# Kernel tuning notes

Hardware: AMD Instinct MI355X
Metric: run time of the kernel (lower is better)

## Reference

```python
import jax, jax.numpy as jnp
import numpy as np

GROUP_SIZES = [2048, 4096, 8192, 16384]
TOP_K = 64
L1_COEFF = 1e-3
AUX_PENALTY = 1e-2
N_BATCHES_TO_DEAD = 20
AUX_K_MULT = 16


def setup_inputs() -> dict:
    D = 1024
    S = sum(GROUP_SIZES)  # 30720
    B = 2048
    key = jax.random.key(0)
    k1, k2, k3 = jax.random.split(key, 3)
    x = jax.random.normal(k1, (B, D), dtype=jnp.float32)
    # kaiming_uniform-like init for W_enc [D, S]
    bound = np.sqrt(6.0 / D)
    W_enc = jax.random.uniform(k2, (D, S), jnp.float32, -bound, bound)
    # W_dec = W_enc.T row-normalized (as in __init__)
    W_dec = W_enc.T
    W_dec = W_dec / jnp.linalg.norm(W_dec, axis=-1, keepdims=True)
    b_dec = jnp.zeros((D,), jnp.float32)
    b_enc = jnp.zeros((S,), jnp.float32)
    num_batches_not_active = jax.random.randint(k3, (S,), 0, 40, dtype=jnp.int32)
    return dict(x=x, b_dec=b_dec, b_enc=b_enc, W_enc=W_enc, W_dec=W_dec,
                num_batches_not_active=num_batches_not_active)


def reference(x, b_dec, b_enc, W_enc, W_dec, num_batches_not_active):
    B, D = x.shape
    S = W_enc.shape[1]
    # encoder
    acts = jax.nn.relu((x - b_dec) @ W_enc + b_enc)  # [B, S]
    # global (batch-level) top-k over flattened activations + scatter back
    k = TOP_K * B
    flat = acts.reshape(-1)
    vals, idx = jax.lax.top_k(flat, k)
    acts_topk = jnp.zeros_like(flat).at[idx].set(vals).reshape(B, S)
    # hierarchical group-wise decode with per-group L2 losses
    bounds = np.concatenate([[0], np.cumsum(GROUP_SIZES)]).astype(int)
    recon = jnp.broadcast_to(b_dec, (B, D))
    l2_losses = []
    for i in range(len(GROUP_SIZES)):
        s, e = int(bounds[i]), int(bounds[i + 1])
        recon = recon + acts_topk[:, s:e] @ W_dec[s:e, :]
        l2_losses.append(jnp.mean((recon - x) ** 2))
    mean_l2_loss = jnp.mean(jnp.stack(l2_losses))
    l1_loss = L1_COEFF * jnp.mean(jnp.sum(jnp.abs(acts_topk), axis=-1))
    # auxiliary dead-feature loss
    dead = num_batches_not_active >= N_BATCHES_TO_DEAD  # [S] bool
    residual = jax.lax.stop_gradient(x - recon)
    k_aux = TOP_K * AUX_K_MULT * B  # assumes num_dead * B >= k_aux (holds here)
    masked = jnp.where(dead[None, :], acts, -jnp.inf)
    min_top_k_val = jax.lax.top_k(masked.reshape(-1), k_aux)[0][-1]
    min_top_k_val = jnp.where(jnp.isfinite(min_top_k_val), min_top_k_val, 0.0)
    acts_aux = jax.nn.relu(acts - min_top_k_val) * dead[None, :].astype(acts.dtype)
    recon_aux = acts_aux @ W_dec  # dead-only contribution (others zeroed)
    aux_loss = AUX_PENALTY * jnp.mean((recon_aux - residual) ** 2)
    aux_loss = jnp.where(jnp.any(dead), aux_loss, 0.0)
    total_loss = mean_l2_loss + l1_loss + aux_loss
    l0_norm = jnp.mean(jnp.sum((acts_topk > 0).astype(jnp.float32), axis=-1))
    return total_loss, mean_l2_loss, l1_loss, aux_loss, l0_norm, acts_topk, recon
```

## Files before the change

kernel.cpp:

```cpp
#include <hip/hip_runtime.h>

#define NB 2048
#define ND 1024
#define NS 30720
#define K_MAIN 131072LL
#define K_AUX  2097152LL
#define BAND_CAP 16384
#define SEL_CAP  8192
#define CANDA_CAP 65536
#define EPS_BAND 1e-3f
#define KSPLIT 4

#define OFF_SCAL 0
#define OFF_ACC  256
#define OFF_H1M  512
#define OFF_H1A  16896
#define OFF_H2M  33280
#define OFF_H2A  49664
#define OFF_ZERO_END 66048
#define OFF_DEAD 66048
#define OFF_SEL_IDX 98304
#define OFF_SEL_BITS 131072
#define OFF_BANDI 163840
#define OFF_BANDV 229376
#define OFF_CAB  360448
#define OFF_RAUX 1048576ULL
#define OFF_AH   (OFF_RAUX + (unsigned long long)KSPLIT * NB * ND * 4)
#define OFF_AL   (OFF_AH + 2048ULL*1024*2)
#define OFF_WHT  (OFF_AL + 2048ULL*1024*2)
#define OFF_WLT  (OFF_WHT + 30720ULL*1024*2)
#define WS_NEED_ENC (OFF_WLT + 30720ULL*1024*2)
#define OFF_AXB  OFF_AH
#define OFF_WDT  (OFF_AXB + 2048ULL*30720*2)
#define WS_NEED_AUX (OFF_WDT + 1024ULL*30720*2)

#define S_NDEAD 0
#define S_B1M 1
#define S_REM1M 2
#define S_B1A 3
#define S_REM1A 4
#define S_T24M 5
#define S_BLO 6
#define S_BHI 7
#define S_T24A 8
#define S_JA 9
#define S_NHI 10
#define S_BANDC 11
#define S_CCA 12
#define S_SELCNT 13
#define S_L0 14
#define S_MINBITS 15

#define A_L2_0 0
#define A_L1 4
#define A_AUX 5

typedef __attribute__((ext_vector_type(8))) short bf16x8;
typedef __attribute__((ext_vector_type(4))) float f32x4;

__device__ __forceinline__ float blk_reduce(float v, float* sred) {
    int t = threadIdx.x;
    #pragma unroll
    for (int o = 32; o > 0; o >>= 1) v += __shfl_down(v, o, 64);
    __syncthreads();
    if ((t & 63) == 0) sred[t >> 6] = v;
    __syncthreads();
    return sred[0] + sred[1] + sred[2] + sred[3];
}

__device__ __forceinline__ unsigned short f2bf(float f) {
    unsigned u = __float_as_uint(f);
    unsigned r = (u + 0x7FFFu + ((u >> 16) & 1u)) >> 16;
    return (unsigned short)r;
}
__device__ __forceinline__ float bf2f(unsigned short h) {
    return __uint_as_float(((unsigned)h) << 16);
}

#define GLD16(gp, lp) __builtin_amdgcn_global_load_lds( \
    (const __attribute__((address_space(1))) unsigned int*)(gp), \
    (__attribute__((address_space(3))) unsigned int*)(lp), 16, 0, 0)

__global__ void k_init(int* w) {
    int n = OFF_ZERO_END / 4;
    for (int i = blockIdx.x * blockDim.x + threadIdx.x; i < n; i += gridDim.x * blockDim.x)
        w[i] = 0;
}

__global__ void k_dead(const int* __restrict__ nbna, unsigned char* __restrict__ dead, int* scal) {
    int stride = gridDim.x * blockDim.x;
    int cnt = 0;
    for (int i = blockIdx.x * blockDim.x + threadIdx.x; i < NS; i += stride) {
        bool d = nbna[i] >= 20;
        dead[i] = d ? 1 : 0;
        cnt += d ? 1 : 0;
    }
    #pragma unroll
    for (int o = 32; o > 0; o >>= 1) cnt += __shfl_down(cnt, o, 64);
    if ((threadIdx.x & 63) == 0 && cnt) atomicAdd(&scal[S_NDEAD], cnt);
}

__global__ void k_prep_a(const float* __restrict__ x, const float* __restrict__ b_dec,
                         unsigned short* __restrict__ Ahg, unsigned short* __restrict__ Alg) {
    int stride = gridDim.x * blockDim.x;
    for (int i = blockIdx.x * blockDim.x + threadIdx.x; i < NB * ND; i += stride) {
        float v = x[i] - b_dec[i & (ND - 1)];
        unsigned short h = f2bf(v);
        unsigned short l = f2bf(v - bf2f(h));
        Ahg[i] = h; Alg[i] = l;
    }
}

__global__ __launch_bounds__(256) void k_prep_w(const float* __restrict__ W,
        unsigned short* __restrict__ WhT, unsigned short* __restrict__ WlT) {
    __shared__ float tile[32][33];
    int n0 = blockIdx.x * 32, k0 = blockIdx.y * 32;
    int t = threadIdx.x;
    int c = t & 31, r = t >> 5;
    #pragma unroll
    for (int it = 0; it < 4; it++)
        tile[r + it * 8][c] = W[(size_t)(k0 + r + it * 8) * NS + n0 + c];
    __syncthreads();
    int kl = t & 31, nl = t >> 5;
    #pragma unroll
    for (int it = 0; it < 4; it++) {
        float v = tile[kl][nl + it * 8];
        unsigned short h = f2bf(v);
        unsigned short l = f2bf(v - bf2f(h));
        size_t o = (size_t)(n0 + nl + it * 8) * ND + k0 + kl;
        WhT[o] = h; WlT[o] = l;
    }
}

#define ENC_STAGE(bufoff, p, gptr, r, ktn) GLD16((gptr) + (size_t)(r) * 128 * ND + (size_t)(ktn) * 32, \
    smem + (bufoff) + (p) * 8192 + (r) * 4096 + ldsw)

__global__ __launch_bounds__(512, 2) void k_enc_mfma(
        const unsigned short* __restrict__ Ahg, const unsigned short* __restrict__ Alg,
        const unsigned short* __restrict__ WhT, const unsigned short* __restrict__ WlT,
        const float* __restrict__ b_enc, float* __restrict__ acts) {
    __shared__ unsigned short smem[65536];
    const int t = threadIdx.x;
    const int lane = t & 63, w = t >> 6;
    const int wm = w >> 2, wn = w & 3;
    const int flat = blockIdx.x;
    const int wg = (flat & 7) * 120 + (flat >> 3);
    const int n0 = (wg >> 3) * 256;
    const int m0 = (wg & 7) * 256;
    const int ln15 = lane & 15, q = lane >> 4;
    const int cph8 = ((q ^ ((lane >> 1) & 3)) << 3);

    const int srow = w * 16 + (lane >> 2);
    const int sq8 = (((lane & 3) ^ ((lane >> 3) & 3)) << 3);
    const unsigned short* gA  = Ahg + (size_t)(m0 + srow) * ND + sq8;
    const unsigned short* gAl = Alg + (size_t)(m0 + srow) * ND + sq8;
    const unsigned short* gB  = WhT + (size_t)(n0 + srow) * ND + sq8;
    const unsigned short* gBl = WlT + (size_t)(n0 + srow) * ND + sq8;
    const int ldsw = w * 512;

    f32x4 acc[8][4];
    #pragma unroll
    for (int i = 0; i < 8; i++)
        #pragma unroll
        for (int j = 0; j < 4; j++) acc[i][j] = (f32x4){0.f, 0.f, 0.f, 0.f};

    ENC_STAGE(0, 0, gA, 0, 0);  ENC_STAGE(0, 0, gA, 1, 0);
    ENC_STAGE(0, 1, gAl, 0, 0); ENC_STAGE(0, 1, gAl, 1, 0);
    ENC_STAGE(0, 2, gB, 0, 0);  ENC_STAGE(0, 2, gB, 1, 0);
    ENC_STAGE(0, 3, gBl, 0, 0); ENC_STAGE(0, 3, gBl, 1, 0);
    asm volatile("s_waitcnt vmcnt(0)" ::: "memory");
    __builtin_amdgcn_s_barrier();
    __builtin_amdgcn_sched_barrier(0);

    const int arb = wm * 128 + ln15;
    const int brb = wn * 64 + ln15;

    for (int kt = 0; kt < 32; ++kt) {
        const int cboff = (kt & 1) * 32768;
        const int nboff = ((kt + 1) & 1) * 32768;
        const int kn = kt + 1;
        const bool more = kn < 32;

        bf16x8 ah[8], bh[4], al[8], bl[4];

        #pragma unroll
        for (int i = 0; i < 8; i++)
            ah[i] = *(const bf16x8*)&smem[cboff + (arb + i * 16) * 32 + cph8];
        #pragma unroll
        for (int j = 0; j < 4; j++)
            bh[j] = *(const bf16x8*)&smem[cboff + 2 * 8192 + (brb + j * 16) * 32 + cph8];
        if (more) {
            ENC_STAGE(nboff, 0, gA, 0, kn);  ENC_STAGE(nboff, 0, gA, 1, kn);
            ENC_STAGE(nboff, 1, gAl, 0, kn); ENC_STAGE(nboff, 1, gAl, 1, kn);
        }
        __builtin_amdgcn_s_barrier();
        asm volatile("s_waitcnt lgkmcnt(0)" ::: "memory");
        __builtin_amdgcn_s_setprio(1);
        #pragma unroll
        for (int i = 0; i < 8; i++)
            #pragma unroll
            for (int j = 0; j < 4; j++)
                acc[i][j] = __builtin_amdgcn_mfma_f32_16x16x32_bf16(ah[i], bh[j], acc[i][j], 0, 0, 0);
        __builtin_amdgcn_s_setprio(0);
        __builtin_amdgcn_s_barrier();

        #pragma unroll
        for (int j = 0; j < 4; j++)
            bl[j] = *(const bf16x8*)&smem[cboff + 3 * 8192 + (brb + j * 16) * 32 + cph8];
        if (more) {
            ENC_STAGE(nboff, 2, gB, 0, kn);  ENC_STAGE(nboff, 2, gB, 1, kn);
            ENC_STAGE(nboff, 3, gBl, 0, kn); ENC_STAGE(nboff, 3, gBl, 1, kn);
        }
        __builtin_amdgcn_s_barrier();
        asm volatile("s_waitcnt lgkmcnt(0)" ::: "memory");
        __builtin_amdgcn_s_setprio(1);
        #pragma unroll
        for (int i = 0; i < 8; i++)
            #pragma unroll
            for (int j = 0; j < 4; j++)
                acc[i][j] = __builtin_amdgcn_mfma_f32_16x16x32_bf16(ah[i], bl[j], acc[i][j], 0, 0, 0);
        __builtin_amdgcn_s_setprio(0);
        __builtin_amdgcn_s_barrier();

        #pragma unroll
        for (int i = 0; i < 8; i++)
            al[i] = *(const bf16x8*)&smem[cboff + 8192 + (arb + i * 16) * 32 + cph8];
        __builtin_amdgcn_s_barrier();
        asm volatile("s_waitcnt lgkmcnt(0)" ::: "memory");
        __builtin_amdgcn_s_setprio(1);
        #pragma unroll
        for (int i = 0; i < 8; i++)
            #pragma unroll
            for (int j = 0; j < 4; j++)
                acc[i][j] = __builtin_amdgcn_mfma_f32_16x16x32_bf16(al[i], bh[j], acc[i][j], 0, 0, 0);
        __builtin_amdgcn_s_setprio(0);
        asm volatile("s_waitcnt vmcnt(0)" ::: "memory");
        __builtin_amdgcn_s_barrier();
        __builtin_amdgcn_sched_barrier(0);
    }

    #pragma unroll
    for (int j = 0; j < 4; j++) {
        int n = n0 + wn * 64 + j * 16 + ln15;
        float be = b_enc[n];
        #pragma unroll
        for (int i = 0; i < 8; i++) {
            int mrow = m0 + wm * 128 + i * 16 + q * 4;
            #pragma unroll
            for (int rg = 0; rg < 4; rg++)
                acts[(size_t)(mrow + rg) * NS + n] = fmaxf(acc[i][j][rg] + be, 0.f);
        }
    }
}

#define GBM 128
#define GBN 128
#define GBK 8
__global__ __launch_bounds__(256) void k_enc_gemm(const float* __restrict__ x,
        const float* __restrict__ b_dec, const float* __restrict__ b_enc,
        const float* __restrict__ W, float* __restrict__ acts) {
    __shared__ float As[GBK][GBM];
    __shared__ float Bs[GBK][GBN];
    const int t = threadIdx.x;
    const int tx = t & 15, ty = t >> 4;
    const int m0 = blockIdx.y * GBM, n0 = blockIdx.x * GBN;
    const int am = t >> 1, ak = (t & 1) * 4;
    const int bk = t >> 5, bnq = (t & 31) * 4;
    float acc[8][8];
    #pragma unroll
    for (int i = 0; i < 8; i++)
        #pragma unroll
        for (int j = 0; j < 8; j++) acc[i][j] = 0.f;
    for (int k0 = 0; k0 < ND; k0 += GBK) {
        float4 av = *(const float4*)(x + (size_t)(m0 + am) * ND + k0 + ak);
        float4 bd = *(const float4*)(b_dec + k0 + ak);
        As[ak + 0][am] = av.x - bd.x;
        As[ak + 1][am] = av.y - bd.y;
        As[ak + 2][am] = av.z - bd.z;
        As[ak + 3][am] = av.w - bd.w;
        *(float4*)&Bs[bk][bnq] = *(const float4*)(W + (size_t)(k0 + bk) * NS + n0 + bnq);
        __syncthreads();
        #pragma unroll
        for (int kk = 0; kk < GBK; kk++) {
            float a[8], b[8];
            *(float4*)&a[0] = *(const float4*)&As[kk][ty * 4];
            *(float4*)&a[4] = *(const float4*)&As[kk][64 + ty * 4];
            *(float4*)&b[0] = *(const float4*)&Bs[kk][tx * 4];
            *(float4*)&b[4] = *(const float4*)&Bs[kk][64 + tx * 4];
            #pragma unroll
            for (int i = 0; i < 8; i++)
                #pragma unroll
                for (int j = 0; j < 8; j++)
                    acc[i][j] = fmaf(a[i], b[j], acc[i][j]);
        }
        __syncthreads();
    }
    float be[8];
    #pragma unroll
    for (int j = 0; j < 4; j++) {
        be[j]     = b_enc[n0 + tx * 4 + j];
        be[4 + j] = b_enc[n0 + 64 + tx * 4 + j];
    }
    #pragma unroll
    for (int i = 0; i < 8; i++) {
        int row = m0 + ((i < 4) ? (ty * 4 + i) : (64 + ty * 4 + i - 4));
        float* orow = acts + (size_t)row * NS + n0;
        #pragma unroll
        for (int j = 0; j < 4; j++) {
            orow[tx * 4 + j]      = fmaxf(acc[i][j] + be[j], 0.f);
            orow[64 + tx * 4 + j] = fmaxf(acc[i][4 + j] + be[4 + j], 0.f);
        }
    }
}

__global__ __launch_bounds__(256) void k_hist1(const float* __restrict__ acts,
        const unsigned char* __restrict__ dead, int* h1m, int* h1a) {
    __shared__ int hm[4096], ha[4096];
    int t = threadIdx.x;
    for (int i = t; i < 4096; i += 256) { hm[i] = 0; ha[i] = 0; }
    __syncthreads();
    for (int row = blockIdx.x; row < NB; row += gridDim.x) {
        const float* pr = acts + (size_t)row * NS;
        for (int c = t; c < NS; c += 256) {
            unsigned bits = __float_as_uint(pr[c]);
            bool isz = (bits == 0u);
            bool dd = dead[c] != 0;
            unsigned long long mz = __ballot(isz);
            unsigned long long mza = __ballot(isz && dd);
            if ((t & 63) == 0) {
                int nz = __popcll(mz);
                if (nz) atomicAdd(&hm[0], nz);
                int nza = __popcll(mza);
                if (nza) atomicAdd(&ha[0], nza);
            }
            if (!isz) {
                atomicAdd(&hm[bits >> 20], 1);
                if (dd) atomicAdd(&ha[bits >> 20], 1);
            }
        }
    }
    __syncthreads();
    for (int i = t; i < 4096; i += 256) {
        if (hm[i]) atomicAdd(&h1m[i], hm[i]);
        if (ha[i]) atomicAdd(&h1a[i], ha[i]);
    }
}

__global__ void k_scan(const int* __restrict__ hist, int* scal, int mode) {
    __shared__ long long csum[256];
    __shared__ long long totsh;
    int t = threadIdx.x;
    int base = t * 16;
    int h[16];
    long long loc = 0;
    #pragma unroll
    for (int i = 0; i < 16; i++) { h[i] = hist[base + i]; loc += h[i]; }
    csum[t] = loc;
    __syncthreads();
    if (t == 0) {
        long long run = 0;
        for (int c = 255; c >= 0; c--) { long long tmp = csum[c]; csum[c] = run; run += tmp; }
        totsh = run;
    }
    __syncthreads();
    long long k;
    if (mode == 0) k = K_MAIN;
    else if (mode == 1) k = K_AUX;
    else if (mode == 2) k = (long long)scal[S_REM1M];
    else {
        if (scal[S_B1A] < 0) { if (t == 0) { scal[S_T24A] = -1; scal[S_MINBITS] = 0; } return; }
        k = (long long)scal[S_REM1A];
    }
    if (mode == 1 && k > totsh) { if (t == 0) scal[S_B1A] = -1; return; }
    long long cum = csum[t];
    int fb = -1; long long rem = 0;
    for (int i = 15; i >= 0; i--) {
        long long ca = cum;
        cum += h[i];
        if (ca < k && k <= cum) { fb = base + i; rem = k - ca; }
    }
    if (fb >= 0) {
        if (mode == 0)      { scal[S_B1M] = fb; scal[S_REM1M] = (int)rem; }
        else if (mode == 1) { scal[S_B1A] = fb; scal[S_REM1A] = (int)rem; }
        else if (mode == 2) {
            int t24 = (scal[S_B1M] << 12) | fb;
            scal[S_T24M] = t24;
            float center = __uint_as_float((((unsigned)t24) << 8) | 128u);
            float lo = center - EPS_BAND;
            if (lo < 0.f) lo = 0.f;
            scal[S_BLO] = (int)__float_as_uint(lo);
            scal[S_BHI] = (int)__float_as_uint(center + EPS_BAND);
        }
        else { scal[S_T24A] = (scal[S_B1A] << 12) | fb; scal[S_JA] = (int)rem; }
    }
}

__global__ __launch_bounds__(256) void k_hist2(const float* __restrict__ acts,
        const unsigned char* __restrict__ dead, const int* scal, int* h2m, int* h2a) {
    int b1m = scal[S_B1M], b1a = scal[S_B1A];
    int row = blockIdx.x, t = threadIdx.x;
    const float* pr = acts + (size_t)row * NS;
    for (int c = t; c < NS; c += 256) {
        unsigned bits = __float_as_uint(pr[c]);
        int hi = (int)(bits >> 20);
        if (hi == b1m) atomicAdd(&h2m[(bits >> 8) & 0xFFF], 1);
        if (b1a >= 0 && hi == b1a && dead[c]) atomicAdd(&h2a[(bits >> 8) & 0xFFF], 1);
    }
}

__global__ __launch_bounds__(256) void k_collect(const float* __restrict__ acts,
        const unsigned char* __restrict__ dead, int* scal,
        int* bandi, unsigned* cab) {
    int row = blockIdx.x, t = threadIdx.x;
    unsigned blo = (unsigned)scal[S_BLO], bhi = (unsigned)scal[S_BHI];
    int t24a = scal[S_T24A];
    const float* pr = acts + (size_t)row * NS;
    int cnt = 0;
    for (int c = t; c < NS; c += 256) {
        unsigned bits = __float_as_uint(pr[c]);
        if (bits > bhi) cnt++;
        else if (bits >= blo) {
            int p = atomicAdd(&scal[S_BANDC], 1);
            if (p < BAND_CAP) bandi[p] = row * NS + c;
        }
        if (t24a >= 0 && (bits >> 8) == (unsigned)t24a && dead[c]) {
            int p = atomicAdd(&scal[S_CCA], 1);
            if (p < CANDA_CAP) cab[p] = bits;
        }
    }
    #pragma unroll
    for (int o = 32; o > 0; o >>= 1) cnt += __shfl_down(cnt, o, 64);
    __shared__ int s2[4];
    if ((t & 63) == 0) s2[t >> 6] = cnt;
    __syncthreads();
    if (t == 0) {
        int tot = s2[0] + s2[1] + s2[2] + s2[3];
        if (tot) atomicAdd(&scal[S_NHI], tot);
    }
}

__global__ __launch_bounds__(256) void k_resolve(const unsigned* __restrict__ cab, int* scal) {
    __shared__ int h[256];
    int t = threadIdx.x;
    h[t] = 0;
    __syncthreads();
    int t24a = scal[S_T24A];
    if (t24a < 0) { if (t == 0) scal[S_MINBITS] = 0; return; }
    int cnt = min(scal[S_CCA], CANDA_CAP);
    int ja = scal[S_JA];
    for (int e = t; e < cnt; e += 256) atomicAdd(&h[cab[e] & 0xFF], 1);
    __syncthreads();
    if (t == 0) {
        long long cum = 0; int L = 0;
        for (int b = 255; b >= 0; b--) {
            long long ca = cum; cum += h[b];
            if (ca < ja && ja <= cum) { L = b; break; }
        }
        scal[S_MINBITS] = (int)((((unsigned)t24a) << 8) | (unsigned)L);
    }
}

__global__ __launch_bounds__(256) void k_band_re(const float* __restrict__ x,
        const float* __restrict__ b_dec, const float* __restrict__ b_enc,
        const float* __restrict__ W, const int* scal,
        const int* __restrict__ bandi, double* __restrict__ bandv) {
    int n = min(scal[S_BANDC], BAND_CAP);
    int t = threadIdx.x;
    __shared__ double sd[4];
    for (int e = blockIdx.x; e < n; e += gridDim.x) {
        int idx = bandi[e];
        int r = idx / NS, c = idx - r * NS;
        double s = 0.0;
        #pragma unroll
        for (int j = 0; j < 4; j++) {
            int d = t + j * 256;
            s += ((double)x[(size_t)r * ND + d] - (double)b_dec[d]) * (double)W[(size_t)d * NS + c];
        }
        #pragma unroll
        for (int o = 32; o > 0; o >>= 1) s += __shfl_down(s, o, 64);
        if ((t & 63) == 0) sd[t >> 6] = s;
        __syncthreads();
        if (t == 0) {
            double v = sd[0] + sd[1] + sd[2] + sd[3] + (double)b_enc[c];
            bandv[e] = fmax(v, 0.0);
        }
        __syncthreads();
    }
}

__global__ __launch_bounds__(256) void k_band_sel(int* scal,
        const int* __restrict__ bandi, const double* __restrict__ bandv,
        int* sel_idx, unsigned* sel_bits) {
    int n = min(scal[S_BANDC], BAND_CAP);
    int need = (int)(K_MAIN - (long long)scal[S_NHI]);
    if (need < 0) need = 0;
    if (need > n) need = n;
    int t = threadIdx.x;
    for (int e = t; e < n; e += 256) {
        double v = bandv[e];
        int idx = bandi[e];
        int rank = 0;
        for (int j = 0; j < n; j++) {
            double vj = bandv[j];
            rank += (vj > v || (vj == v && bandi[j] < idx)) ? 1 : 0;
        }
        if (rank < need) {
            int p = atomicAdd(&scal[S_SELCNT], 1);
            if (p < SEL_CAP) { sel_idx[p] = idx; sel_bits[p] = __float_as_uint((float)v); }
        }
    }
}

__global__ __launch_bounds__(256) void k_decode(const float* __restrict__ acts,
        const float* __restrict__ x, const float* __restrict__ b_dec, const float* __restrict__ Wd,
        float* __restrict__ recon, const int* scal,
        const int* __restrict__ sel_idx, double* acc) {
    int row = blockIdx.x, t = threadIdx.x;
    unsigned blo = (unsigned)scal[S_BLO], bhi = (unsigned)scal[S_BHI];
    int selcnt = min(scal[S_SELCNT], SEL_CAP);
    __shared__ int lj[2048];
    __shared__ float lv[2048];
    __shared__ int lcnt;
    __shared__ float sred[4];
    const int d0 = t * 4;
    float4 r;
    r.x = b_dec[d0]; r.y = b_dec[d0 + 1]; r.z = b_dec[d0 + 2]; r.w = b_dec[d0 + 3];
    float4 xv = *(const float4*)(x + (size_t)row * ND + d0);
    const float* arow = acts + (size_t)row * NS;
    const int bnds[5] = {0, 2048, 6144, 14336, NS};
    for (int g = 0; g < 4; g++) {
        for (int c0 = bnds[g]; c0 < bnds[g + 1]; c0 += 2048) {
            __syncthreads();
            if (t == 0) lcnt = 0;
            __syncthreads();
            #pragma unroll
            for (int u = 0; u < 8; u++) {
                int c = c0 + u * 256 + t;
                float v = arow[c];
                unsigned bits = __float_as_uint(v);
                bool keep = bits > bhi;
                if (!keep && bits >= blo) {
                    int flat = row * NS + c;
                    for (int e = 0; e < selcnt; e++)
                        if (sel_idx[e] == flat) { keep = true; break; }
                }
                if (keep) { int p = atomicAdd(&lcnt, 1); lj[p] = c; lv[p] = v; }
            }
            __syncthreads();
            int n = lcnt;
            for (int e = 0; e < n; e++) {
                float a_ = lv[e];
                float4 w = *(const float4*)(Wd + (size_t)lj[e] * ND + d0);
                r.x = fmaf(a_, w.x, r.x);
                r.y = fmaf(a_, w.y, r.y);
                r.z = fmaf(a_, w.z, r.z);
                r.w = fmaf(a_, w.w, r.w);
            }
        }
        float dx = r.x - xv.x, dy = r.y - xv.y, dz = r.z - xv.z, dw = r.w - xv.w;
        float ss = dx * dx + dy * dy + dz * dz + dw * dw;
        float tot = blk_reduce(ss, sred);
        if (t == 0) atomicAdd(&acc[A_L2_0 + g], (double)tot);
    }
    float* orow = recon + (size_t)row * ND + d0;
    orow[0] = r.x; orow[1] = r.y; orow[2] = r.z; orow[3] = r.w;
}

__global__ __launch_bounds__(256) void k_aux_pack(const float* __restrict__ acts,
        const unsigned char* __restrict__ dead, const int* scal,
        unsigned short* __restrict__ axb) {
    int row = blockIdx.x, t = threadIdx.x;
    float minval = __uint_as_float((unsigned)scal[S_MINBITS]);
    const float* arow = acts + (size_t)row * NS;
    unsigned short* orow = axb + (size_t)row * NS;
    for (int c = t; c < NS; c += 256) {
        float v = arow[c];
        float o = (dead[c] && v > minval) ? (v - minval) : 0.f;
        orow[c] = f2bf(o);
    }
}

__global__ __launch_bounds__(256) void k_prep_wd(const float* __restrict__ Wd,
        unsigned short* __restrict__ WdT) {
    __shared__ float tile[32][33];
    int s0 = blockIdx.x * 32, d0 = blockIdx.y * 32;
    int t = threadIdx.x;
    int c = t & 31, r = t >> 5;
    #pragma unroll
    for (int it = 0; it < 4; it++)
        tile[r + it * 8][c] = Wd[(size_t)(s0 + r + it * 8) * ND + d0 + c];
    __syncthreads();
    int sl = t & 31, dl = t >> 5;
    #pragma unroll
    for (int it = 0; it < 4; it++)
        WdT[(size_t)(d0 + dl + it * 8) * NS + s0 + sl] = f2bf(tile[sl][dl + it * 8]);
}

__global__ __launch_bounds__(256) void k_aux_mfma(
        const unsigned short* __restrict__ axb, const unsigned short* __restrict__ WdT,
        float* __restrict__ raux) {
    __shared__ unsigned short As[128 * 32], Bs[128 * 32];
    const int t = threadIdx.x;
    const int lane = t & 63, w = t >> 6;
    const int wm = w >> 1, wn = w & 1;
    const int m0 = blockIdx.y * 128, n0 = blockIdx.x * 128;
    const int kbase = blockIdx.z * (NS / KSPLIT);
    const int ln15 = lane & 15, q = lane >> 4;

    f32x4 acc[4][4];
    #pragma unroll
    for (int i = 0; i < 4; i++)
        #pragma unroll
        for (int j = 0; j < 4; j++) acc[i][j] = (f32x4){0.f, 0.f, 0.f, 0.f};

    const unsigned short* gbase;
    unsigned short* lbase;
    if (w < 2) { gbase = axb + (size_t)(m0 + w * 64) * NS; lbase = As + w * 64 * 32; }
    else       { gbase = WdT + (size_t)(n0 + (w - 2) * 64) * NS; lbase = Bs + (w - 2) * 64 * 32; }
    const unsigned short* glane = gbase + (size_t)(lane >> 2) * NS + (lane & 3) * 8 + kbase;

    for (int k0 = 0; k0 < NS / KSPLIT; k0 += 32) {
        __syncthreads();
        #pragma unroll
        for (int ch = 0; ch < 4; ch++)
            GLD16(glane + (size_t)ch * 16 * NS + k0, lbase + ch * 512);
        __syncthreads();

        bf16x8 af[4];
        #pragma unroll
        for (int i = 0; i < 4; i++)
            af[i] = *(const bf16x8*)&As[(wm * 64 + i * 16 + ln15) * 32 + q * 8];
        #pragma unroll
        for (int j = 0; j < 4; j++) {
            bf16x8 bf = *(const bf16x8*)&Bs[(wn * 64 + j * 16 + ln15) * 32 + q * 8];
            #pragma unroll
            for (int i = 0; i < 4; i++)
                acc[i][j] = __builtin_amdgcn_mfma_f32_16x16x32_bf16(af[i], bf, acc[i][j], 0, 0, 0);
        }
    }
    float* rz = raux + (size_t)blockIdx.z * NB * ND;
    #pragma unroll
    for (int j = 0; j < 4; j++) {
        int n = n0 + wn * 64 + j * 16 + ln15;
        #pragma unroll
        for (int i = 0; i < 4; i++) {
            int mrow = m0 + wm * 64 + i * 16 + q * 4;
            #pragma unroll
            for (int rg = 0; rg < 4; rg++)
                rz[(size_t)(mrow + rg) * ND + n] = acc[i][j][rg];
        }
    }
}

__global__ __launch_bounds__(256) void k_aux_diff(const float* __restrict__ raux,
        const float* __restrict__ x, const float* __restrict__ recon, double* acc) {
    __shared__ float sred[4];
    float ss = 0.f;
    int stride = gridDim.x * blockDim.x;
    for (int i = blockIdx.x * blockDim.x + threadIdx.x; i < NB * ND; i += stride) {
        float ra = raux[i];
        #pragma unroll
        for (int z = 1; z < KSPLIT; z++) ra += raux[(size_t)z * NB * ND + i];
        float d = ra - (x[i] - recon[i]);
        ss += d * d;
    }
    float tot = blk_reduce(ss, sred);
    if (threadIdx.x == 0) atomicAdd(&acc[A_AUX], (double)tot);
}

__global__ __launch_bounds__(256) void k_aux(const float* __restrict__ acts,
        const unsigned char* __restrict__ dead, const float* __restrict__ x,
        const float* __restrict__ recon, const float* __restrict__ Wd,
        const int* scal, double* acc) {
    int row = blockIdx.x, t = threadIdx.x;
    float minval = __uint_as_float((unsigned)scal[S_MINBITS]);
    __shared__ int lj[2048];
    __shared__ float lv[2048];
    __shared__ int lcnt;
    __shared__ float sred[4];
    float4 r = {0.f, 0.f, 0.f, 0.f};
    const float* arow = acts + (size_t)row * NS;
    const int d0 = t * 4;
    for (int c0 = 0; c0 < NS; c0 += 2048) {
        __syncthreads();
        if (t == 0) lcnt = 0;
        __syncthreads();
        #pragma unroll
        for (int u = 0; u < 8; u++) {
            int c = c0 + u * 256 + t;
            float v = arow[c];
            if (dead[c] && v > minval) {
                int p = atomicAdd(&lcnt, 1);
                lj[p] = c; lv[p] = v - minval;
            }
        }
        __syncthreads();
        int n = lcnt;
        for (int e = 0; e < n; e++) {
            float a_ = lv[e];
            float4 w = *(const float4*)(Wd + (size_t)lj[e] * ND + d0);
            r.x = fmaf(a_, w.x, r.x);
            r.y = fmaf(a_, w.y, r.y);
            r.z = fmaf(a_, w.z, r.z);
            r.w = fmaf(a_, w.w, r.w);
        }
    }
    const float* xr = x + (size_t)row * ND + d0;
    const float* rr = recon + (size_t)row * ND + d0;
    float dx = r.x - (xr[0] - rr[0]);
    float dy = r.y - (xr[1] - rr[1]);
    float dz = r.z - (xr[2] - rr[2]);
    float dw = r.w - (xr[3] - rr[3]);
    float ss = dx * dx + dy * dy + dz * dz + dw * dw;
    float tot = blk_reduce(ss, sred);
    if (t == 0) atomicAdd(&acc[A_AUX], (double)tot);
}

__global__ __launch_bounds__(256) void k_topk_write(float* __restrict__ out, const int* scal, double* acc, int* scalw) {
    unsigned bhi = (unsigned)scal[S_BHI];
    float l1 = 0.f;
    int cnt = 0;
    const long long vstart = 8, nvec = 15728639;
    long long stride = (long long)gridDim.x * blockDim.x;
    for (long long i = (long long)blockIdx.x * blockDim.x + threadIdx.x; i < nvec; i += stride) {
        float4* p = (float4*)(out + vstart) + i;
        float4 v = *p;
        #define PROC(F) { unsigned b = __float_as_uint(v.F); if (b > bhi) { l1 += v.F; cnt++; } else v.F = 0.f; }
        PROC(x) PROC(y) PROC(z) PROC(w)
        #undef PROC
        *p = v;
    }
    if (blockIdx.x == 0 && threadIdx.x == 0) {
        const long long head[4] = {5, 6, 7, 62914564LL};
        for (int q = 0; q < 4; q++) {
            float v = out[head[q]];
            unsigned b = __float_as_uint(v);
            if (b > bhi) { l1 += v; cnt++; } else out[head[q]] = 0.f;
        }
    }
    int t = threadIdx.x;
    #pragma unroll
    for (int o = 32; o > 0; o >>= 1) { l1 += __shfl_down(l1, o, 64); cnt += __shfl_down(cnt, o, 64); }
    __shared__ float s1[4];
    __shared__ int s2[4];
    if ((t & 63) == 0) { s1[t >> 6] = l1; s2[t >> 6] = cnt; }
    __syncthreads();
    if (t == 0) {
        atomicAdd(&acc[A_L1], (double)(s1[0] + s1[1] + s1[2] + s1[3]));
        atomicAdd(&scalw[S_L0], s2[0] + s2[1] + s2[2] + s2[3]);
    }
}

__global__ __launch_bounds__(256) void k_selwrite(float* __restrict__ acts, const int* __restrict__ sel_idx,
        const unsigned* __restrict__ sel_bits, int* scal, double* acc) {
    int t = threadIdx.x;
    int n = min(scal[S_SELCNT], SEL_CAP);
    float l1 = 0.f;
    for (int e = t; e < n; e += 256) {
        float v = __uint_as_float(sel_bits[e]);
        acts[sel_idx[e]] = v;
        l1 += v;
    }
    #pragma unroll
    for (int o = 32; o > 0; o >>= 1) l1 += __shfl_down(l1, o, 64);
    __shared__ float s1[4];
    if ((t & 63) == 0) s1[t >> 6] = l1;
    __syncthreads();
    if (t == 0) {
        atomicAdd(&acc[A_L1], (double)(s1[0] + s1[1] + s1[2] + s1[3]));
        atomicAdd(&scal[S_L0], n);
    }
}

__global__ void k_final(float* out, const int* scal, const double* acc) {
    if (threadIdx.x == 0 && blockIdx.x == 0) {
        double ml2 = (acc[0] + acc[1] + acc[2] + acc[3]) * 0.25 / ((double)NB * ND);
        double l1 = 1e-3 * acc[A_L1] / (double)NB;
        double aux = (scal[S_NDEAD] > 0) ? (1e-2 * acc[A_AUX] / ((double)NB * ND)) : 0.0;
        out[0] = (float)(ml2 + l1 + aux);
        out[1] = (float)ml2;
        out[2] = (float)l1;
        out[3] = (float)aux;
        out[4] = (float)scal[S_L0] / (float)NB;
    }
}

extern "C" void kernel_launch(void* const* d_in, const int* in_sizes, int n_in,
                              void* d_out, int out_size, void* d_ws, size_t ws_size,
                              hipStream_t stream) {
    const float* x     = (const float*)d_in[0];
    const float* b_dec = (const float*)d_in[1];
    const float* b_enc = (const float*)d_in[2];
    const float* W_enc = (const float*)d_in[3];
    const float* W_dec = (const float*)d_in[4];
    const int*   nbna  = (const int*)d_in[5];

    float* out = (float*)d_out;
    float* acts  = out + 5;
    float* recon = out + 5 + (size_t)NB * NS;

    char* ws = (char*)d_ws;
    int*    scal = (int*)(ws + OFF_SCAL);
    double* acc  = (double*)(ws + OFF_ACC);
    int*    h1m  = (int*)(ws + OFF_H1M);
    int*    h1a  = (int*)(ws + OFF_H1A);
    int*    h2m  = (int*)(ws + OFF_H2M);
    int*    h2a  = (int*)(ws + OFF_H2A);
    unsigned char* dead = (unsigned char*)(ws + OFF_DEAD);
    int*      sel_idx  = (int*)(ws + OFF_SEL_IDX);
    unsigned* sel_bits = (unsigned*)(ws + OFF_SEL_BITS);
    int*      bandi = (int*)(ws + OFF_BANDI);
    double*   bandv = (double*)(ws + OFF_BANDV);
    unsigned* cab   = (unsigned*)(ws + OFF_CAB);
    float*    raux  = (float*)(ws + OFF_RAUX);
    unsigned short* Ahg = (unsigned short*)(ws + OFF_AH);
    unsigned short* Alg = (unsigned short*)(ws + OFF_AL);
    unsigned short* WhT = (unsigned short*)(ws + OFF_WHT);
    unsigned short* WlT = (unsigned short*)(ws + OFF_WLT);
    unsigned short* axb = (unsigned short*)(ws + OFF_AXB);
    unsigned short* WdT = (unsigned short*)(ws + OFF_WDT);

    const bool use_mfma     = (ws_size >= WS_NEED_ENC);
    const bool use_aux_gemm = (ws_size >= WS_NEED_AUX);

    k_init<<<64, 256, 0, stream>>>((int*)d_ws);
    k_dead<<<60, 256, 0, stream>>>(nbna, dead, scal);
    if (use_mfma) {
        k_prep_a<<<512, 256, 0, stream>>>(x, b_dec, Ahg, Alg);
        k_prep_w<<<dim3(NS / 32, ND / 32), 256, 0, stream>>>(W_enc, WhT, WlT);
        k_enc_mfma<<<(NB / 256) * (NS / 256), 512, 0, stream>>>(Ahg, Alg, WhT, WlT, b_enc, acts);
    } else {
        k_enc_gemm<<<dim3(NS / GBN, NB / GBM), 256, 0, stream>>>(x, b_dec, b_enc, W_enc, acts);
    }
    k_hist1<<<1024, 256, 0, stream>>>(acts, dead, h1m, h1a);
    k_scan<<<1, 256, 0, stream>>>(h1m, scal, 0);
    k_scan<<<1, 256, 0, stream>>>(h1a, scal, 1);
    k_hist2<<<NB, 256, 0, stream>>>(acts, dead, scal, h2m, h2a);
    k_scan<<<1, 256, 0, stream>>>(h2m, scal, 2);
    k_scan<<<1, 256, 0, stream>>>(h2a, scal, 3);
    k_collect<<<NB, 256, 0, stream>>>(acts, dead, scal, bandi, cab);
    k_resolve<<<1, 256, 0, stream>>>(cab, scal);
    k_band_re<<<512, 256, 0, stream>>>(x, b_dec, b_enc, W_enc, scal, bandi, bandv);
    k_band_sel<<<1, 256, 0, stream>>>(scal, bandi, bandv, sel_idx, sel_bits);
    k_decode<<<NB, 256, 0, stream>>>(acts, x, b_dec, W_dec, recon, scal, sel_idx, acc);
    if (use_aux_gemm) {
        k_aux_pack<<<NB, 256, 0, stream>>>(acts, dead, scal, axb);
        k_prep_wd<<<dim3(NS / 32, ND / 32), 256, 0, stream>>>(W_dec, WdT);
        k_aux_mfma<<<dim3(ND / 128, NB / 128, KSPLIT), 256, 0, stream>>>(axb, WdT, raux);
        k_aux_diff<<<512, 256, 0, stream>>>(raux, x, recon, acc);
    } else {
        k_aux<<<NB, 256, 0, stream>>>(acts, dead, x, recon, W_dec, scal, acc);
    }
    k_topk_write<<<4096, 256, 0, stream>>>(out, scal, acc, scal);
    k_selwrite<<<1, 256, 0, stream>>>(acts, sel_idx, sel_bits, scal, acc);
    k_final<<<1, 64, 0, stream>>>(out, scal, acc);
}
```

Before: 2.069 ms.

## Software-pipeline encoder MFMA loop with partial vmcnt waits and peeled final iteration

Reorders the encoder GEMM main loop so the next tile's global-to-LDS loads are issued before the current tile's LDS reads and MFMAs. The full vmcnt(0) drain and several barriers per K-step are replaced by partial vmcnt waits. The last K iteration is peeled so the loop body needs no guard. The goal is to hide global load latency behind MFMA work and cut synchronisation stalls. The cost is more fragile buffer-reuse reasoning across waves, since the double buffer is now overwritten with fewer barriers.

```diff
diff --git a/kernel.cpp b/kernel.cpp
--- a/kernel.cpp
+++ b/kernel.cpp
@@ -135,6 +135,24 @@
 #define ENC_STAGE(bufoff, p, gptr, r, ktn) GLD16((gptr) + (size_t)(r) * 128 * ND + (size_t)(ktn) * 32, \
     smem + (bufoff) + (p) * 8192 + (r) * 4096 + ldsw)
 
+#define ENC_RD_AH(boff) { _Pragma("unroll") \
+    for (int i = 0; i < 8; i++) ah[i] = *(const bf16x8*)&smem[(boff) + (arb + i * 16) * 32 + cph8]; }
+#define ENC_RD_BH(boff) { _Pragma("unroll") \
+    for (int j = 0; j < 4; j++) bh[j] = *(const bf16x8*)&smem[(boff) + 2 * 8192 + (brb + j * 16) * 32 + cph8]; }
+#define ENC_RD_BL(boff) { _Pragma("unroll") \
+    for (int j = 0; j < 4; j++) bl[j] = *(const bf16x8*)&smem[(boff) + 3 * 8192 + (brb + j * 16) * 32 + cph8]; }
+#define ENC_RD_AL(boff) { _Pragma("unroll") \
+    for (int i = 0; i < 8; i++) al[i] = *(const bf16x8*)&smem[(boff) + 8192 + (arb + i * 16) * 32 + cph8]; }
+
+#define ENC_MFMA(AF, BF) { \
+    asm volatile("s_waitcnt lgkmcnt(0)" ::: "memory"); \
+    __builtin_amdgcn_sched_barrier(0); \
+    __builtin_amdgcn_s_setprio(1); \
+    _Pragma("unroll") for (int i = 0; i < 8; i++) \
+        _Pragma("unroll") for (int j = 0; j < 4; j++) \
+            acc[i][j] = __builtin_amdgcn_mfma_f32_16x16x32_bf16(AF[i], BF[j], acc[i][j], 0, 0, 0); \
+    __builtin_amdgcn_s_setprio(0); }
+
 __global__ __launch_bounds__(512, 2) void k_enc_mfma(
         const unsigned short* __restrict__ Ahg, const unsigned short* __restrict__ Alg,
         const unsigned short* __restrict__ WhT, const unsigned short* __restrict__ WlT,
@@ -164,79 +182,51 @@
         #pragma unroll
         for (int j = 0; j < 4; j++) acc[i][j] = (f32x4){0.f, 0.f, 0.f, 0.f};
 
+    const int arb = wm * 128 + ln15;
+    const int brb = wn * 64 + ln15;
+
     ENC_STAGE(0, 0, gA, 0, 0);  ENC_STAGE(0, 0, gA, 1, 0);
-    ENC_STAGE(0, 1, gAl, 0, 0); ENC_STAGE(0, 1, gAl, 1, 0);
     ENC_STAGE(0, 2, gB, 0, 0);  ENC_STAGE(0, 2, gB, 1, 0);
     ENC_STAGE(0, 3, gBl, 0, 0); ENC_STAGE(0, 3, gBl, 1, 0);
-    asm volatile("s_waitcnt vmcnt(0)" ::: "memory");
-    __builtin_amdgcn_s_barrier();
-    __builtin_amdgcn_sched_barrier(0);
-
-    const int arb = wm * 128 + ln15;
-    const int brb = wn * 64 + ln15;
-
-    for (int kt = 0; kt < 32; ++kt) {
+    ENC_STAGE(0, 1, gAl, 0, 0); ENC_STAGE(0, 1, gAl, 1, 0);
+
+    for (int kt = 0; kt < 31; ++kt) {
         const int cboff = (kt & 1) * 32768;
-        const int nboff = ((kt + 1) & 1) * 32768;
+        const int nboff = cboff ^ 32768;
         const int kn = kt + 1;
-        const bool more = kn < 32;
-
-        bf16x8 ah[8], bh[4], al[8], bl[4];
-
-        #pragma unroll
-        for (int i = 0; i < 8; i++)
-            ah[i] = *(const bf16x8*)&smem[cboff + (arb + i * 16) * 32 + cph8];
-        #pragma unroll
-        for (int j = 0; j < 4; j++)
-            bh[j] = *(const bf16x8*)&smem[cboff + 2 * 8192 + (brb + j * 16) * 32 + cph8];
-        if (more) {
-            ENC_STAGE(nboff, 0, gA, 0, kn);  ENC_STAGE(nboff, 0, gA, 1, kn);
-            ENC_STAGE(nboff, 1, gAl, 0, kn); ENC_STAGE(nboff, 1, gAl, 1, kn);
-        }
+        bf16x8 ah[8], bh[4], bl[4], al[8];
+
+        ENC_STAGE(nboff, 0, gA, 0, kn);  ENC_STAGE(nboff, 0, gA, 1, kn);
+        ENC_STAGE(nboff, 2, gB, 0, kn);  ENC_STAGE(nboff, 2, gB, 1, kn);
+        asm volatile("s_waitcnt vmcnt(8)" ::: "memory");
         __builtin_amdgcn_s_barrier();
-        asm volatile("s_waitcnt lgkmcnt(0)" ::: "memory");
-        __builtin_amdgcn_s_setprio(1);
-        #pragma unroll
-        for (int i = 0; i < 8; i++)
-            #pragma unroll
-            for (int j = 0; j < 4; j++)
-                acc[i][j] = __builtin_amdgcn_mfma_f32_16x16x32_bf16(ah[i], bh[j], acc[i][j], 0, 0, 0);
-        __builtin_amdgcn_s_setprio(0);
+        ENC_RD_AH(cboff) ENC_RD_BH(cboff)
+        ENC_MFMA(ah, bh)
+
+        ENC_STAGE(nboff, 3, gBl, 0, kn); ENC_STAGE(nboff, 3, gBl, 1, kn);
+        ENC_STAGE(nboff, 1, gAl, 0, kn); ENC_STAGE(nboff, 1, gAl, 1, kn);
+        asm volatile("s_waitcnt vmcnt(8)" ::: "memory");
         __builtin_amdgcn_s_barrier();
-
-        #pragma unroll
-        for (int j = 0; j < 4; j++)
-            bl[j] = *(const bf16x8*)&smem[cboff + 3 * 8192 + (brb + j * 16) * 32 + cph8];
-        if (more) {
-            ENC_STAGE(nboff, 2, gB, 0, kn);  ENC_STAGE(nboff, 2, gB, 1, kn);
-            ENC_STAGE(nboff, 3, gBl, 0, kn); ENC_STAGE(nboff, 3, gBl, 1, kn);
-        }
+        ENC_RD_BL(cboff)
+        ENC_MFMA(ah, bl)
+
+        ENC_RD_AL(cboff)
+        ENC_MFMA(al, bh)
+    }
+
+    {
+        const int cboff = 32768;
+        bf16x8 ah[8], bh[4], bl[4], al[8];
+        asm volatile("s_waitcnt vmcnt(4)" ::: "memory");
         __builtin_amdgcn_s_barrier();
-        asm volatile("s_waitcnt lgkmcnt(0)" ::: "memory");
-        __builtin_amdgcn_s_setprio(1);
-        #pragma unroll
-        for (int i = 0; i < 8; i++)
-            #pragma unroll
-            for (int j = 0; j < 4; j++)
-                acc[i][j] = __builtin_amdgcn_mfma_f32_16x16x32_bf16(ah[i], bl[j], acc[i][j], 0, 0, 0);
-        __builtin_amdgcn_s_setprio(0);
-        __builtin_amdgcn_s_barrier();
-
-        #pragma unroll
-        for (int i = 0; i < 8; i++)
-            al[i] = *(const bf16x8*)&smem[cboff + 8192 + (arb + i * 16) * 32 + cph8];
-        __builtin_amdgcn_s_barrier();
-        asm volatile("s_waitcnt lgkmcnt(0)" ::: "memory");
-        __builtin_amdgcn_s_setprio(1);
-        #pragma unroll
-        for (int i = 0; i < 8; i++)
-            #pragma unroll
-            for (int j = 0; j < 4; j++)
-                acc[i][j] = __builtin_amdgcn_mfma_f32_16x16x32_bf16(al[i], bh[j], acc[i][j], 0, 0, 0);
-        __builtin_amdgcn_s_setprio(0);
+        ENC_RD_AH(cboff) ENC_RD_BH(cboff)
+        ENC_MFMA(ah, bh)
         asm volatile("s_waitcnt vmcnt(0)" ::: "memory");
         __builtin_amdgcn_s_barrier();
-        __builtin_amdgcn_sched_barrier(0);
+        ENC_RD_BL(cboff)
+        ENC_MFMA(ah, bl)
+        ENC_RD_AL(cboff)
+        ENC_MFMA(al, bh)
     }
 
     #pragma unroll
```

New measurement: 2.029 ms. About the same (-1.9%).
